# Kernel optimization log

Hardware: AMD Instinct MI355X
Metric: run time of the kernel (lower is better)

Reference implementation:

```python
import jax, jax.numpy as jnp
import numpy as np

B, N, D, H, S = 64, 1000, 512, 8, 20
DK = D // H
TANH_CLIP = 10.0
NEG = -1e9


def setup_inputs() -> dict:
    key = jax.random.key(0)
    k1, k2, k3, k4, k5 = jax.random.split(key, 5)
    embeddings = jax.random.normal(k1, (B, N, D), dtype=jnp.float32)
    q = jax.random.normal(k2, (B, S, D), dtype=jnp.float32)
    # action_mask: True = feasible. Ensure at least one feasible node per row.
    action_mask = jax.random.bernoulli(k3, 0.5, (B, S, N))
    action_mask = action_mask.at[:, :, 0].set(True)
    W_kvl = jax.random.normal(k4, (D, 3 * D), dtype=jnp.float32) * (1.0 / np.sqrt(D))
    W_out = jax.random.normal(k5, (D, D), dtype=jnp.float32) * (1.0 / np.sqrt(D))
    return {"embeddings": embeddings, "q": q, "action_mask": action_mask,
            "W_kvl": W_kvl, "W_out": W_out}


def reference(embeddings, q, action_mask, W_kvl, W_out):
    # _precompute: project node embeddings into glimpse K, V and logit K
    kvl = jnp.einsum('bnd,de->bne', embeddings, W_kvl)  # [B,N,3D]
    glimpse_k, glimpse_v, logit_k = jnp.split(kvl, 3, axis=-1)
    # dynamic embedding is zero (StaticEmbedding for TSP)

    mask = ~action_mask  # True = infeasible, shape [B,S,N]

    # multi-head glimpse attention
    qh = q.reshape(B, S, H, DK)
    kh = glimpse_k.reshape(B, N, H, DK)
    vh = glimpse_v.reshape(B, N, H, DK)
    compat = jnp.einsum('bshd,bnhd->bhsn', qh, kh) / np.sqrt(DK)
    compat = jnp.where(mask[:, None, :, :], NEG, compat)
    attn = jax.nn.softmax(compat, axis=-1)
    heads = jnp.einsum('bhsn,bnhd->bshd', attn, vh).reshape(B, S, D)
    glimpse = jnp.einsum('bsd,de->bse', heads, W_out)  # [B,S,D]

    # pointer logits against logit_k, tanh clipping, mask, log-softmax
    logits = jnp.einsum('bsd,bnd->bsn', glimpse, logit_k) / np.sqrt(D)
    logits = TANH_CLIP * jnp.tanh(logits)
    logits = jnp.where(mask, NEG, logits)
    log_p = jax.nn.log_softmax(logits, axis=-1)  # [B,S,N]

    # rearrange 'b s l -> (s b) l'
    return jnp.swapaxes(log_p, 0, 1).reshape(S * B, N)
```

## Files before the change

kernel.cpp:

```cpp
#include <hip/hip_runtime.h>

#define BB 64
#define NN 1000
#define NP 1024
#define DD 512
#define HH 8
#define SS 20
#define NEGV -1e9f

typedef float v4f __attribute__((ext_vector_type(4)));
typedef short v8s __attribute__((ext_vector_type(8)));
typedef int   v8i __attribute__((ext_vector_type(8)));
typedef int   v4i __attribute__((ext_vector_type(4)));
typedef unsigned char uchar;
typedef unsigned long long ulong_t;

static __device__ __forceinline__ short f2bf(float f) {
    unsigned u = __builtin_bit_cast(unsigned, f);
    u = (u + 0x7fffu + ((u >> 16) & 1u)) >> 16;
    return (short)u;
}
static __device__ __forceinline__ float bf2f(short s) {
    unsigned u = ((unsigned)(unsigned short)s) << 16;
    return __builtin_bit_cast(float, u);
}
static __device__ __forceinline__ uchar f2fp8(float f) {
    return (uchar)(__builtin_amdgcn_cvt_pk_fp8_f32(f, 0.f, 0, false) & 0xff);
}

static __device__ __forceinline__ void gld16(const void* g, void* l) {
    __builtin_amdgcn_global_load_lds(
        (const __attribute__((address_space(1))) void*)(g),
        (__attribute__((address_space(3))) void*)(l),
        16, 0, 0);
}

__global__ void prep(const float* __restrict__ Wkvl, uchar* __restrict__ Wt8,
                     const float* __restrict__ Wout, short* __restrict__ Wot,
                     const float* __restrict__ emb, int* __restrict__ emb8) {
    __shared__ float t[32][33];
    int bid = blockIdx.x, tid = threadIdx.x;
    if (bid < 768) {
        int c0 = (bid % 48) * 32, r0 = (bid / 48) * 32;
        int x = tid & 31, y = tid >> 5;
        for (int k = 0; k < 32; k += 8)
            t[y + k][x] = Wkvl[(long)(r0 + y + k) * 1536 + c0 + x];
        __syncthreads();
        for (int k = 0; k < 32; k += 8)
            Wt8[(long)(c0 + y + k) * 512 + r0 + x] = f2fp8(t[x][y + k]);
    } else if (bid < 1024) {
        int bb = bid - 768;
        int c0 = (bb & 15) * 32, r0 = (bb >> 4) * 32;
        int x = tid & 31, y = tid >> 5;
        for (int k = 0; k < 32; k += 8)
            t[y + k][x] = Wout[(long)(r0 + y + k) * 512 + c0 + x];
        __syncthreads();
        for (int k = 0; k < 32; k += 8)
            Wot[(long)(c0 + y + k) * 512 + r0 + x] = f2bf(t[x][y + k]);
    } else {
        int i = (bid - 1024) * 256 + tid;
        long o = (long)i * 8;
        v4f a = *(const v4f*)(emb + o);
        v4f b = *(const v4f*)(emb + o + 4);
        int lo = __builtin_amdgcn_cvt_pk_fp8_f32(a.x, a.y, 0, false);
        lo = __builtin_amdgcn_cvt_pk_fp8_f32(a.z, a.w, lo, true);
        int hi = __builtin_amdgcn_cvt_pk_fp8_f32(b.x, b.y, 0, false);
        hi = __builtin_amdgcn_cvt_pk_fp8_f32(b.z, b.w, hi, true);
        int2 r; r.x = lo; r.y = hi;
        *(int2*)(emb8 + i * 2) = r;
    }
}

__global__ __launch_bounds__(512) void gemm_kvl(const uchar* __restrict__ emb8,
                                                const uchar* __restrict__ Wt8,
                                                uchar* __restrict__ kvl8) {
    extern __shared__ __align__(16) uchar smem[];
    uchar* As0 = smem;
    uchar* Bs0 = smem + 32768;
    int tid = threadIdx.x;
    int id = blockIdx.x;
    int wgid = (id & 7) * 750 + (id >> 3);
    int m_idx = wgid / 12, n_idx = wgid - m_idx * 12;
    int m0 = m_idx * 128, n0 = n_idx * 128;
    int wid = tid >> 6, lane = tid & 63, quad = lane >> 4, l16 = lane & 15;
    int wm = wid & 1, wn = wid >> 1;
    const uchar* Ag = emb8 + (long)m0 * 512;
    const uchar* Bg = Wt8 + (long)n0 * 512;
    int rsub = lane >> 3;
    int kc = ((lane & 7) ^ rsub) * 16;

    v4f acc[4][2] = {};

    auto stageAB = [&](int bi, int kk) {
        #pragma unroll
        for (int p = 0; p < 2; ++p) {
            int rl = wid * 16 + p * 8;
            gld16(Ag + (long)(rl + rsub) * 512 + kk + kc, As0 + bi * 16384 + rl * 128);
        }
        #pragma unroll
        for (int p = 0; p < 2; ++p) {
            int rl = wid * 16 + p * 8;
            gld16(Bg + (long)(rl + rsub) * 512 + kk + kc, Bs0 + bi * 16384 + rl * 128);
        }
    };
    auto ldfrag = [&](const uchar* base, int row) -> v8i {
        int c0 = (quad * 2) ^ (row & 7);
        v4i lo = *(const v4i*)(base + row * 128 + c0 * 16);
        v4i hi = *(const v4i*)(base + row * 128 + (c0 ^ 1) * 16);
        return __builtin_shufflevector(lo, hi, 0, 1, 2, 3, 4, 5, 6, 7);
    };

    stageAB(0, 0);
    stageAB(1, 128);
    asm volatile("s_waitcnt vmcnt(4)" ::: "memory");
    __builtin_amdgcn_s_barrier();
    __builtin_amdgcn_sched_barrier(0);

    v8i af[4], bf[2];
    #pragma unroll
    for (int t = 0; t < 4; ++t) {
        int cur = t & 1;
        const uchar* ab = As0 + cur * 16384;
        const uchar* bb = Bs0 + cur * 16384;
        #pragma unroll
        for (int i = 0; i < 4; ++i) af[i] = ldfrag(ab, wm * 64 + i * 16 + l16);
        #pragma unroll
        for (int j = 0; j < 2; ++j) bf[j] = ldfrag(bb, wn * 32 + j * 16 + l16);
        __builtin_amdgcn_s_setprio(1);
        #pragma unroll
        for (int i = 0; i < 4; ++i)
            acc[i][0] = __builtin_amdgcn_mfma_scale_f32_16x16x128_f8f6f4(
                af[i], bf[0], acc[i][0], 0, 0, 0, 0x7f7f7f7f, 0, 0x7f7f7f7f);
        __builtin_amdgcn_s_setprio(0);
        asm volatile("s_waitcnt lgkmcnt(0)" ::: "memory");
        __builtin_amdgcn_s_barrier();
        if (t < 2) stageAB(cur, (t + 2) * 128);
        __builtin_amdgcn_s_setprio(1);
        #pragma unroll
        for (int i = 0; i < 4; ++i)
            acc[i][1] = __builtin_amdgcn_mfma_scale_f32_16x16x128_f8f6f4(
                af[i], bf[1], acc[i][1], 0, 0, 0, 0x7f7f7f7f, 0, 0x7f7f7f7f);
        __builtin_amdgcn_s_setprio(0);
        if (t < 3) {
            if (t < 2) asm volatile("s_waitcnt vmcnt(4)" ::: "memory");
            else       asm volatile("s_waitcnt vmcnt(0)" ::: "memory");
            __builtin_amdgcn_s_barrier();
            __builtin_amdgcn_sched_barrier(0);
        }
    }
    __syncthreads();

    short* rp = (short*)smem;
    short* r = rp + wid * (16 * 40);
    int nw = n0 + wn * 32;
    #pragma unroll
    for (int i = 0; i < 4; ++i) {
        #pragma unroll
        for (int jj = 0; jj < 2; ++jj)
            #pragma unroll
            for (int rr = 0; rr < 4; ++rr)
                r[(quad * 4 + rr) * 40 + jj * 16 + l16] = f2bf(acc[i][jj][rr]);
        {
            int rowl = lane >> 2;
            int colc = (lane & 3) * 8;
            v8s val = *(const v8s*)(r + rowl * 40 + colc);
            int lo = __builtin_amdgcn_cvt_pk_fp8_f32(bf2f(val[0]), bf2f(val[1]), 0, false);
            lo = __builtin_amdgcn_cvt_pk_fp8_f32(bf2f(val[2]), bf2f(val[3]), lo, true);
            int hi = __builtin_amdgcn_cvt_pk_fp8_f32(bf2f(val[4]), bf2f(val[5]), 0, false);
            hi = __builtin_amdgcn_cvt_pk_fp8_f32(bf2f(val[6]), bf2f(val[7]), hi, true);
            int2 st; st.x = lo; st.y = hi;
            *(int2*)(kvl8 + (long)(m0 + wm * 64 + i * 16 + rowl) * 1536 +
                     nw + colc) = st;
        }
    }
}

#define CST 1036
__global__ __launch_bounds__(512) void attn_fused(const float* __restrict__ q,
                                                  const uchar* __restrict__ kvl8,
                                                  const int* __restrict__ mask,
                                                  float* __restrict__ heads) {
    extern __shared__ __align__(16) uchar asm_[];
    uchar* qs = asm_;
    short* cmp = (short*)(asm_ + 2304);
    uchar* vscr = (uchar*)cmp;
    uchar* VfL = asm_ + 43744;
    int b = blockIdx.x, h = blockIdx.y;
    int tid = threadIdx.x, wid = tid >> 6, lane = tid & 63, quad = lane >> 4, l16 = lane & 15;

    for (int i = tid; i < 32 * 64; i += 512) {
        int row = i >> 6, col = i & 63;
        float v = (row < SS) ? q[((long)b * SS + row) * DD + h * 64 + col] : 0.f;
        qs[row * 72 + col] = f2fp8(v);
    }

    {
        int gsub = tid >> 8;
        int t2 = tid & 255;
        int node_l = t2 >> 2, chunk = (t2 & 3) * 16;
        int wid2 = t2 >> 6, lane2 = t2 & 63, l162 = lane2 & 15, quad2 = lane2 >> 4;
        uchar* VT = vscr + gsub * 4608;
        for (int gg = 0; gg < 8; ++gg) {
            int g = gg * 2 + gsub;
            int gn = g * 64 + node_l;
            int ncl = gn < NN ? gn : NN - 1;
            const uchar* vp = kvl8 + ((long)b * NN + ncl) * 1536 + 512 + h * 64 + chunk;
            ulong_t v0 = *(const ulong_t*)(vp);
            ulong_t v1 = *(const ulong_t*)(vp + 8);
            uchar* b0p = (uchar*)&v0; uchar* b1p = (uchar*)&v1;
            #pragma unroll
            for (int j = 0; j < 8; ++j) VT[(chunk + j) * 72 + node_l] = b0p[j];
            #pragma unroll
            for (int j = 0; j < 8; ++j) VT[(chunk + 8 + j) * 72 + node_l] = b1p[j];
            __syncthreads();
            #pragma unroll
            for (int sub = 0; sub < 2; ++sub) {
                ulong_t frag = *(const ulong_t*)&VT[(wid2 * 16 + l162) * 72 + sub * 32 + quad2 * 8];
                *(ulong_t*)(VfL + ((wid2 * 32) + (g * 2 + sub)) * 512 + lane2 * 8) = frag;
            }
            __syncthreads();
        }
    }

    long af[2][2];
    #pragma unroll
    for (int mt = 0; mt < 2; ++mt)
        #pragma unroll
        for (int ks = 0; ks < 2; ++ks)
            af[mt][ks] = *(const long*)(qs + (mt * 16 + l16) * 72 + ks * 32 + quad * 8);
    for (int t = 0; t < 8; ++t) {
        int nt = wid * 8 + t;
        int n = nt * 16 + l16;
        int nc = n < NN ? n : NN - 1;
        const uchar* kp = kvl8 + ((long)b * NN + nc) * 1536 + h * 64 + quad * 8;
        long b0 = *(const long*)kp;
        long b1 = *(const long*)(kp + 32);
        #pragma unroll
        for (int mt = 0; mt < 2; ++mt) {
            v4f a = {};
            a = __builtin_amdgcn_mfma_f32_16x16x32_fp8_fp8(af[mt][0], b0, a, 0, 0, 0);
            a = __builtin_amdgcn_mfma_f32_16x16x32_fp8_fp8(af[mt][1], b1, a, 0, 0, 0);
            #pragma unroll
            for (int r = 0; r < 4; ++r) {
                int s = mt * 16 + quad * 4 + r;
                if (s < SS) cmp[s * CST + nt * 16 + l16] = f2bf(a[r] * 0.125f);
            }
        }
    }
    __syncthreads();
    for (int s = wid; s < SS; s += 8) {
        const int* mr = mask + ((long)b * SS + s) * NN;
        float x[16];
        float mx = NEGV;
        #pragma unroll
        for (int i = 0; i < 16; ++i) {
            int n = lane + 64 * i;
            float v = bf2f(cmp[s * CST + n]);
            bool feas = (n < NN) && (mr[n < NN ? n : 0] != 0);
            x[i] = feas ? v : NEGV;
            mx = fmaxf(mx, x[i]);
        }
        for (int off = 32; off; off >>= 1) mx = fmaxf(mx, __shfl_xor(mx, off));
        float sum = 0.f;
        #pragma unroll
        for (int i = 0; i < 16; ++i) { x[i] = __expf(x[i] - mx); sum += x[i]; }
        for (int off = 32; off; off >>= 1) sum += __shfl_xor(sum, off);
        float inv = 1.0f / sum;
        uchar* pr = (uchar*)cmp + (long)s * (CST * 2);
        #pragma unroll
        for (int i = 0; i < 16; ++i) pr[lane + 64 * i] = f2fp8(x[i] * inv);
    }
    __syncthreads();
    int mt = wid & 1, dt = wid >> 1;
    int srow = mt * 16 + l16; if (srow > SS - 1) srow = SS - 1;
    const uchar* ap = (const uchar*)cmp + (long)srow * (CST * 2) + quad * 8;
    const uchar* vfb = VfL + dt * 32 * 512;
    v4f a0 = {}, a1 = {}, a2 = {}, a3 = {};
    for (int k0s = 0; k0s < 32; k0s += 4) {
        a0 = __builtin_amdgcn_mfma_f32_16x16x32_fp8_fp8(
            *(const long*)(ap + k0s * 32),
            *(const long*)(vfb + k0s * 512 + lane * 8), a0, 0, 0, 0);
        a1 = __builtin_amdgcn_mfma_f32_16x16x32_fp8_fp8(
            *(const long*)(ap + (k0s + 1) * 32),
            *(const long*)(vfb + (k0s + 1) * 512 + lane * 8), a1, 0, 0, 0);
        a2 = __builtin_amdgcn_mfma_f32_16x16x32_fp8_fp8(
            *(const long*)(ap + (k0s + 2) * 32),
            *(const long*)(vfb + (k0s + 2) * 512 + lane * 8), a2, 0, 0, 0);
        a3 = __builtin_amdgcn_mfma_f32_16x16x32_fp8_fp8(
            *(const long*)(ap + (k0s + 3) * 32),
            *(const long*)(vfb + (k0s + 3) * 512 + lane * 8), a3, 0, 0, 0);
    }
    v4f accv = (a0 + a1) + (a2 + a3);
    #pragma unroll
    for (int r = 0; r < 4; ++r) {
        int s = mt * 16 + quad * 4 + r;
        if (s < SS)
            heads[((long)b * SS + s) * DD + h * 64 + dt * 16 + l16] = accv[r];
    }
}

__global__ __launch_bounds__(256) void out_proj(const float* __restrict__ heads,
                                                const short* __restrict__ Wot,
                                                float* __restrict__ glimpse) {
    __shared__ __align__(16) short As[64 * 40], Bs[64 * 40];
    int tid = threadIdx.x;
    int m0 = blockIdx.x * 64, n0 = blockIdx.y * 64;
    int wid = tid >> 6, lane = tid & 63, quad = lane >> 4, l16 = lane & 15;
    int wm = wid & 1, wn = wid >> 1;
    int arow = tid >> 3, akol = (tid & 7) * 4;
    int brow = tid >> 2, bkol = (tid & 3) * 8;
    v4f acc[2][2] = {};
    for (int kk = 0; kk < 512; kk += 32) {
        #pragma unroll
        for (int p = 0; p < 2; ++p) {
            int r = arow + p * 32;
            v4f a = *(const v4f*)(heads + (long)(m0 + r) * 512 + kk + akol);
            short4 s4;
            s4.x = f2bf(a.x); s4.y = f2bf(a.y); s4.z = f2bf(a.z); s4.w = f2bf(a.w);
            *(short4*)(As + r * 40 + akol) = s4;
        }
        *(uint4*)(Bs + brow * 40 + bkol) =
            *(const uint4*)(Wot + (long)(n0 + brow) * 512 + kk + bkol);
        __syncthreads();
        #pragma unroll
        for (int i = 0; i < 2; ++i) {
            v8s af = *(const v8s*)(As + (wm * 32 + i * 16 + l16) * 40 + quad * 8);
            #pragma unroll
            for (int j = 0; j < 2; ++j) {
                v8s bf = *(const v8s*)(Bs + (wn * 32 + j * 16 + l16) * 40 + quad * 8);
                acc[i][j] = __builtin_amdgcn_mfma_f32_16x16x32_bf16(af, bf, acc[i][j], 0, 0, 0);
            }
        }
        __syncthreads();
    }
    #pragma unroll
    for (int i = 0; i < 2; ++i)
        #pragma unroll
        for (int j = 0; j < 2; ++j)
            #pragma unroll
            for (int r = 0; r < 4; ++r)
                glimpse[(long)(m0 + wm * 32 + i * 16 + quad * 4 + r) * 512 +
                        n0 + wn * 32 + j * 16 + l16] = acc[i][j][r];
}

__global__ __launch_bounds__(256) void ptr_logits(const float* __restrict__ glimpse,
                                                  const uchar* __restrict__ kvl8,
                                                  float* __restrict__ logits) {
    int b = blockIdx.x, g = blockIdx.y;
    __shared__ __align__(16) uchar Gs[32 * 520];
    int tid = threadIdx.x;
    #pragma unroll
    for (int it = 0; it < 16; ++it) {
        int e = it * 1024 + tid * 4;
        int row = e >> 9, col = e & 511;
        int pk = 0;
        if (row < SS) {
            v4f a = *(const v4f*)(glimpse + ((long)b * SS + row) * 512 + col);
            pk = __builtin_amdgcn_cvt_pk_fp8_f32(a.x, a.y, 0, false);
            pk = __builtin_amdgcn_cvt_pk_fp8_f32(a.z, a.w, pk, true);
        }
        *(int*)(Gs + row * 520 + col) = pk;
    }
    __syncthreads();
    int wid = tid >> 6, lane = tid & 63, quad = lane >> 4, l16 = lane & 15;
    const float scale = 0.04419417382415922f;
    int nt = g * 4 + wid;
    int n = nt * 16 + l16;
    int ncl = n < NN ? n : NN - 1;
    const uchar* kp = kvl8 + ((long)b * NN + ncl) * 1536 + 1024 + quad * 8;
    v4f acc[2] = {};
    for (int k = 0; k < 16; ++k) {
        long bfr = *(const long*)(kp + k * 32);
        #pragma unroll
        for (int m = 0; m < 2; ++m) {
            long afr = *(const long*)(Gs + (m * 16 + l16) * 520 + k * 32 + quad * 8);
            acc[m] = __builtin_amdgcn_mfma_f32_16x16x32_fp8_fp8(afr, bfr, acc[m], 0, 0, 0);
        }
    }
    #pragma unroll
    for (int m = 0; m < 2; ++m)
        #pragma unroll
        for (int r = 0; r < 4; ++r) {
            int s = m * 16 + quad * 4 + r;
            if (s < SS)
                logits[((long)b * SS + s) * NP + nt * 16 + l16] = acc[m][r] * scale;
        }
}

__global__ __launch_bounds__(256) void logsoftmax_out(const float* __restrict__ logits,
                                                      const int* __restrict__ mask,
                                                      float* __restrict__ out) {
    int row = blockIdx.x;
    int b = row / SS, s = row % SS;
    int tid = threadIdx.x;
    __shared__ float red[8];
    int n0 = tid * 4;
    v4f v = *(const v4f*)(logits + (long)row * NP + n0);
    const int* mr = mask + (long)row * NN;
    float x[4];
    float mx = NEGV;
    #pragma unroll
    for (int j = 0; j < 4; ++j) {
        int n = n0 + j;
        float t = 10.f * tanhf(v[j]);
        bool feas = (n < NN) && (mr[n < NN ? n : 0] != 0);
        x[j] = feas ? t : NEGV;
        mx = fmaxf(mx, x[j]);
    }
    for (int off = 32; off; off >>= 1) mx = fmaxf(mx, __shfl_xor(mx, off));
    int wid = tid >> 6, lane = tid & 63;
    if (lane == 0) red[wid] = mx;
    __syncthreads();
    mx = fmaxf(fmaxf(red[0], red[1]), fmaxf(red[2], red[3]));
    float sum = 0.f;
    #pragma unroll
    for (int j = 0; j < 4; ++j) sum += __expf(x[j] - mx);
    for (int off = 32; off; off >>= 1) sum += __shfl_xor(sum, off);
    __syncthreads();
    if (lane == 0) red[4 + wid] = sum;
    __syncthreads();
    sum = red[4] + red[5] + red[6] + red[7];
    float lse = mx + __logf(sum);
    float* orow = out + ((long)s * BB + b) * NN;
    #pragma unroll
    for (int j = 0; j < 4; ++j) {
        int n = n0 + j;
        if (n < NN) orow[n] = x[j] - lse;
    }
}

extern "C" void kernel_launch(void* const* d_in, const int* in_sizes, int n_in,
                              void* d_out, int out_size, void* d_ws, size_t ws_size,
                              hipStream_t stream) {
    const float* emb  = (const float*)d_in[0];
    const float* q    = (const float*)d_in[1];
    const int*   mask = (const int*)d_in[2];
    const float* Wkvl = (const float*)d_in[3];
    const float* Wout = (const float*)d_in[4];
    float* out = (float*)d_out;

    char* ws = (char*)d_ws;
    uchar* kvl8    = (uchar*)ws; ws += (size_t)64000 * 1536;
    uchar* Wt8     = (uchar*)ws; ws += (size_t)1536 * 512;
    uchar* emb8    = (uchar*)ws; ws += (size_t)64000 * 512;
    short* Wot     = (short*)ws; ws += (size_t)512 * 512 * 2;
    float* heads   = (float*)ws; ws += (size_t)BB * SS * DD * 4;
    float* glimpse = (float*)ws; ws += (size_t)BB * SS * DD * 4;
    float* logits  = (float*)ws; ws += (size_t)BB * SS * NP * 4;

    static int s_attr_done = 0;
    if (!s_attr_done) {
        hipFuncSetAttribute(reinterpret_cast<const void*>(gemm_kvl),
                            hipFuncAttributeMaxDynamicSharedMemorySize, 65536);
        hipFuncSetAttribute(reinterpret_cast<const void*>(attn_fused),
                            hipFuncAttributeMaxDynamicSharedMemorySize, 109312);
        s_attr_done = 1;
    }

    prep<<<dim3(1024 + 16000), 256, 0, stream>>>(Wkvl, Wt8, Wout, Wot, emb, (int*)emb8);
    gemm_kvl<<<dim3(6000), 512, 65536, stream>>>(emb8, Wt8, kvl8);
    attn_fused<<<dim3(BB, HH), 512, 109312, stream>>>(q, kvl8, mask, heads);
    out_proj<<<dim3(20, 8), 256, 0, stream>>>(heads, Wot, glimpse);
    ptr_logits<<<dim3(BB, 16), 256, 0, stream>>>(glimpse, kvl8, logits);
    logsoftmax_out<<<dim3(BB * SS), 256, 0, stream>>>(logits, mask, out);
}
```

Baseline: 335.5 us.

## Shrink attention LDS footprint by staging V after softmax in halves

```diff
diff --git a/kernel.cpp b/kernel.cpp
--- a/kernel.cpp
+++ b/kernel.cpp
@@ -183,8 +183,9 @@
     extern __shared__ __align__(16) uchar asm_[];
     uchar* qs = asm_;
     short* cmp = (short*)(asm_ + 2304);
-    uchar* vscr = (uchar*)cmp;
-    uchar* VfL = asm_ + 43744;
+    uchar* VfL = asm_;
+    uchar* vscr = asm_ + 32768;
+    uchar* Pc = asm_ + 45056;
     int b = blockIdx.x, h = blockIdx.y;
     int tid = threadIdx.x, wid = tid >> 6, lane = tid & 63, quad = lane >> 4, l16 = lane & 15;
 
@@ -193,34 +194,7 @@
         float v = (row < SS) ? q[((long)b * SS + row) * DD + h * 64 + col] : 0.f;
         qs[row * 72 + col] = f2fp8(v);
     }
-
-    {
-        int gsub = tid >> 8;
-        int t2 = tid & 255;
-        int node_l = t2 >> 2, chunk = (t2 & 3) * 16;
-        int wid2 = t2 >> 6, lane2 = t2 & 63, l162 = lane2 & 15, quad2 = lane2 >> 4;
-        uchar* VT = vscr + gsub * 4608;
-        for (int gg = 0; gg < 8; ++gg) {
-            int g = gg * 2 + gsub;
-            int gn = g * 64 + node_l;
-            int ncl = gn < NN ? gn : NN - 1;
-            const uchar* vp = kvl8 + ((long)b * NN + ncl) * 1536 + 512 + h * 64 + chunk;
-            ulong_t v0 = *(const ulong_t*)(vp);
-            ulong_t v1 = *(const ulong_t*)(vp + 8);
-            uchar* b0p = (uchar*)&v0; uchar* b1p = (uchar*)&v1;
-            #pragma unroll
-            for (int j = 0; j < 8; ++j) VT[(chunk + j) * 72 + node_l] = b0p[j];
-            #pragma unroll
-            for (int j = 0; j < 8; ++j) VT[(chunk + 8 + j) * 72 + node_l] = b1p[j];
-            __syncthreads();
-            #pragma unroll
-            for (int sub = 0; sub < 2; ++sub) {
-                ulong_t frag = *(const ulong_t*)&VT[(wid2 * 16 + l162) * 72 + sub * 32 + quad2 * 8];
-                *(ulong_t*)(VfL + ((wid2 * 32) + (g * 2 + sub)) * 512 + lane2 * 8) = frag;
-            }
-            __syncthreads();
-        }
-    }
+    __syncthreads();
 
     long af[2][2];
     #pragma unroll
@@ -248,6 +222,7 @@
         }
     }
     __syncthreads();
+
     for (int s = wid; s < SS; s += 8) {
         const int* mr = mask + ((long)b * SS + s) * NN;
         float x[16];
@@ -266,29 +241,60 @@
         for (int i = 0; i < 16; ++i) { x[i] = __expf(x[i] - mx); sum += x[i]; }
         for (int off = 32; off; off >>= 1) sum += __shfl_xor(sum, off);
         float inv = 1.0f / sum;
-        uchar* pr = (uchar*)cmp + (long)s * (CST * 2);
+        uchar* pr = Pc + (long)s * 1040;
         #pragma unroll
         for (int i = 0; i < 16; ++i) pr[lane + 64 * i] = f2fp8(x[i] * inv);
     }
     __syncthreads();
+
     int mt = wid & 1, dt = wid >> 1;
     int srow = mt * 16 + l16; if (srow > SS - 1) srow = SS - 1;
-    const uchar* ap = (const uchar*)cmp + (long)srow * (CST * 2) + quad * 8;
-    const uchar* vfb = VfL + dt * 32 * 512;
+    const uchar* ap = Pc + (long)srow * 1040 + quad * 8;
     v4f a0 = {}, a1 = {}, a2 = {}, a3 = {};
-    for (int k0s = 0; k0s < 32; k0s += 4) {
-        a0 = __builtin_amdgcn_mfma_f32_16x16x32_fp8_fp8(
-            *(const long*)(ap + k0s * 32),
-            *(const long*)(vfb + k0s * 512 + lane * 8), a0, 0, 0, 0);
-        a1 = __builtin_amdgcn_mfma_f32_16x16x32_fp8_fp8(
-            *(const long*)(ap + (k0s + 1) * 32),
-            *(const long*)(vfb + (k0s + 1) * 512 + lane * 8), a1, 0, 0, 0);
-        a2 = __builtin_amdgcn_mfma_f32_16x16x32_fp8_fp8(
-            *(const long*)(ap + (k0s + 2) * 32),
-            *(const long*)(vfb + (k0s + 2) * 512 + lane * 8), a2, 0, 0, 0);
-        a3 = __builtin_amdgcn_mfma_f32_16x16x32_fp8_fp8(
-            *(const long*)(ap + (k0s + 3) * 32),
-            *(const long*)(vfb + (k0s + 3) * 512 + lane * 8), a3, 0, 0, 0);
+    int gsub = tid >> 8;
+    int t2 = tid & 255;
+    int node_l = t2 >> 2, chunk = (t2 & 3) * 16;
+    int wid2 = t2 >> 6, lane2 = t2 & 63, l162 = lane2 & 15, quad2 = lane2 >> 4;
+    uchar* VT = vscr + gsub * 4608;
+    #pragma unroll
+    for (int hf = 0; hf < 2; ++hf) {
+        for (int gg = 0; gg < 4; ++gg) {
+            int gl = gg * 2 + gsub;
+            int gn = (hf * 8 + gl) * 64 + node_l;
+            int ncl = gn < NN ? gn : NN - 1;
+            const uchar* vp = kvl8 + ((long)b * NN + ncl) * 1536 + 512 + h * 64 + chunk;
+            ulong_t v0 = *(const ulong_t*)(vp);
+            ulong_t v1 = *(const ulong_t*)(vp + 8);
+            uchar* b0p = (uchar*)&v0; uchar* b1p = (uchar*)&v1;
+            #pragma unroll
+            for (int j = 0; j < 8; ++j) VT[(chunk + j) * 72 + node_l] = b0p[j];
+            #pragma unroll
+            for (int j = 0; j < 8; ++j) VT[(chunk + 8 + j) * 72 + node_l] = b1p[j];
+            __syncthreads();
+            #pragma unroll
+            for (int sub = 0; sub < 2; ++sub) {
+                ulong_t frag = *(const ulong_t*)&VT[(wid2 * 16 + l162) * 72 + sub * 32 + quad2 * 8];
+                *(ulong_t*)(VfL + ((wid2 * 16) + (gl * 2 + sub)) * 512 + lane2 * 8) = frag;
+            }
+            __syncthreads();
+        }
+        const uchar* vfb = VfL + dt * 16 * 512;
+        for (int k0s = 0; k0s < 16; k0s += 4) {
+            int kg = hf * 16 + k0s;
+            a0 = __builtin_amdgcn_mfma_f32_16x16x32_fp8_fp8(
+                *(const long*)(ap + (kg + 0) * 32),
+                *(const long*)(vfb + (k0s + 0) * 512 + lane * 8), a0, 0, 0, 0);
+            a1 = __builtin_amdgcn_mfma_f32_16x16x32_fp8_fp8(
+                *(const long*)(ap + (kg + 1) * 32),
+                *(const long*)(vfb + (k0s + 1) * 512 + lane * 8), a1, 0, 0, 0);
+            a2 = __builtin_amdgcn_mfma_f32_16x16x32_fp8_fp8(
+                *(const long*)(ap + (kg + 2) * 32),
+                *(const long*)(vfb + (k0s + 2) * 512 + lane * 8), a2, 0, 0, 0);
+            a3 = __builtin_amdgcn_mfma_f32_16x16x32_fp8_fp8(
+                *(const long*)(ap + (kg + 3) * 32),
+                *(const long*)(vfb + (k0s + 3) * 512 + lane * 8), a3, 0, 0, 0);
+        }
+        __syncthreads();
     }
     v4f accv = (a0 + a1) + (a2 + a3);
     #pragma unroll
@@ -453,13 +459,13 @@
         hipFuncSetAttribute(reinterpret_cast<const void*>(gemm_kvl),
                             hipFuncAttributeMaxDynamicSharedMemorySize, 65536);
         hipFuncSetAttribute(reinterpret_cast<const void*>(attn_fused),
-                            hipFuncAttributeMaxDynamicSharedMemorySize, 109312);
+                            hipFuncAttributeMaxDynamicSharedMemorySize, 65856);
         s_attr_done = 1;
     }
 
     prep<<<dim3(1024 + 16000), 256, 0, stream>>>(Wkvl, Wt8, Wout, Wot, emb, (int*)emb8);
     gemm_kvl<<<dim3(6000), 512, 65536, stream>>>(emb8, Wt8, kvl8);
-    attn_fused<<<dim3(BB, HH), 512, 109312, stream>>>(q, kvl8, mask, heads);
+    attn_fused<<<dim3(BB, HH), 512, 65856, stream>>>(q, kvl8, mask, heads);
     out_proj<<<dim3(20, 8), 256, 0, stream>>>(heads, Wot, glimpse);
     ptr_logits<<<dim3(BB, 16), 256, 0, stream>>>(glimpse, kvl8, logits);
     logsoftmax_out<<<dim3(BB * SS), 256, 0, stream>>>(logits, mask, out);
```

After: 325.7 us. 2.9% less time.
